# Optimization experiments

Hardware: AMD Instinct MI355X
Metric: run time of the kernel (lower is better)

## Reference

```python
import jax, jax.numpy as jnp
import numpy as np

EMBED_DIM = 1024
NUM_HEADS = 16
HEAD_DIM = EMBED_DIM // NUM_HEADS
BATCH = 4
SEQ = 2048


def setup_inputs() -> dict:
    key = jax.random.key(0)
    ks = jax.random.split(key, 9)
    s = 1.0 / np.sqrt(EMBED_DIM)
    return {
        "query": jax.random.normal(ks[0], (BATCH, SEQ, EMBED_DIM), jnp.float32),
        "Wq": jax.random.normal(ks[1], (EMBED_DIM, EMBED_DIM), jnp.float32) * s,
        "bq": jnp.zeros((EMBED_DIM,), jnp.float32),
        "Wk": jax.random.normal(ks[2], (EMBED_DIM, EMBED_DIM), jnp.float32) * s,
        "bk": jnp.zeros((EMBED_DIM,), jnp.float32),
        "Wv": jax.random.normal(ks[3], (EMBED_DIM, EMBED_DIM), jnp.float32) * s,
        "bv": jnp.zeros((EMBED_DIM,), jnp.float32),
        "Wo": jax.random.normal(ks[4], (EMBED_DIM, EMBED_DIM), jnp.float32) * s,
        "bo": jnp.zeros((EMBED_DIM,), jnp.float32),
    }


def reference(query, Wq, bq, Wk, bk, Wv, bv, Wo, bo):
    bsz, seq, embed_dim = query.shape
    scaling = HEAD_DIM ** (-0.5)
    # projections (torch Linear: x @ W.T + b)
    q = (query @ Wq.T + bq) * scaling
    k = query @ Wk.T + bk
    v = query @ Wv.T + bv
    # [b, h, s, d]
    q = q.reshape(bsz, seq, NUM_HEADS, HEAD_DIM).transpose(0, 2, 1, 3)
    k = k.reshape(bsz, seq, NUM_HEADS, HEAD_DIM).transpose(0, 2, 1, 3)
    v = v.reshape(bsz, seq, NUM_HEADS, HEAD_DIM).transpose(0, 2, 1, 3)
    # full [b, h, s, s] scores (faithful to the naive original)
    scores = jnp.einsum("bhqd,bhkd->bhqk", q, k)
    causal = jnp.tril(jnp.ones((seq, seq), bool))  # [s, s]
    scores = jnp.where(causal[None, None], scores, -jnp.inf)
    probs = jax.nn.softmax(scores, axis=-1)
    attn = jnp.einsum("bhqk,bhkd->bhqd", probs, v)
    attn = attn.transpose(0, 2, 1, 3).reshape(bsz, seq, embed_dim)
    return attn @ Wo.T + bo
```

## Files before the change

### kernel.cpp

```cpp
#include <hip/hip_runtime.h>
#include <stdint.h>

typedef unsigned short u16;
typedef __attribute__((ext_vector_type(8))) __bf16 bf16x8;
typedef __attribute__((ext_vector_type(4))) float f32x4;

#define SEQL 2048
#define NHEADS 16
#define HDIM 64
#define BSZ 4
#define EMB 1024
#define MROWS (BSZ * SEQL)

__device__ __forceinline__ u16 f2bf(float f) {
  union { float f; uint32_t u; } v; v.f = f;
  return (u16)((v.u + 0x7fffu + ((v.u >> 16) & 1u)) >> 16);
}

__device__ __forceinline__ void gload_lds16(const u16* g, u16* l) {
  __builtin_amdgcn_global_load_lds(
      (__attribute__((address_space(1))) void*)(g),
      (__attribute__((address_space(3))) void*)(l), 16, 0, 0);
}

__device__ __forceinline__ void cvt8(const float* __restrict__ in, u16* __restrict__ out, int i) {
  float4 a = *(const float4*)(in + i);
  float4 b = *(const float4*)(in + i + 4);
  uint4 o;
  o.x = f2bf(a.x) | ((uint32_t)f2bf(a.y) << 16);
  o.y = f2bf(a.z) | ((uint32_t)f2bf(a.w) << 16);
  o.z = f2bf(b.x) | ((uint32_t)f2bf(b.y) << 16);
  o.w = f2bf(b.z) | ((uint32_t)f2bf(b.w) << 16);
  *(uint4*)(out + i) = o;
}

__global__ void cvt_kernel(const float* __restrict__ in, u16* __restrict__ out, int n) {
  int i = (blockIdx.x * blockDim.x + threadIdx.x) * 8;
  if (i + 8 <= n) cvt8(in, out, i);
}

__global__ void cvt_w4(const float* __restrict__ w0, const float* __restrict__ w1,
                       const float* __restrict__ w2, const float* __restrict__ w3,
                       u16* __restrict__ o0, u16* __restrict__ o1,
                       u16* __restrict__ o2, u16* __restrict__ o3) {
  const float* in = blockIdx.y == 0 ? w0 : blockIdx.y == 1 ? w1 : blockIdx.y == 2 ? w2 : w3;
  u16* out = blockIdx.y == 0 ? o0 : blockIdx.y == 1 ? o1 : blockIdx.y == 2 ? o2 : o3;
  int i = (blockIdx.x * blockDim.x + threadIdx.x) * 8;
  cvt8(in, out, i);
}

__device__ __forceinline__ void gemm_core(const u16* __restrict__ A, const u16* __restrict__ B,
                                          int m0, int n0, u16* As, u16* Bs, f32x4 acc[4][4]) {
  const int tid = threadIdx.x;
  const int lane = tid & 63;
  const int wid = tid >> 6;
  const int wm = wid >> 1, wn = wid & 1;
  const int srow = lane >> 2;
  const int scol = (lane & 3) * 8;
  const int lrow = lane & 15;
  const int kg = (lane >> 4) * 8;

  const u16* Ag0 = A + (size_t)(m0 + wid * 32 + srow) * EMB + scol;
  const u16* Bg0 = B + (size_t)(n0 + wid * 32 + srow) * EMB + scol;
  u16* Al0 = As + (wid * 32 + srow) * 32 + scol;
  u16* Bl0 = Bs + (wid * 32 + srow) * 32 + scol;

  for (int k0 = 0; k0 < EMB; k0 += 32) {
    gload_lds16(Ag0 + k0, Al0);
    gload_lds16(Ag0 + k0 + 16 * EMB, Al0 + 16 * 32);
    gload_lds16(Bg0 + k0, Bl0);
    gload_lds16(Bg0 + k0 + 16 * EMB, Bl0 + 16 * 32);
    __syncthreads();
    bf16x8 af[4], bfr[4];
#pragma unroll
    for (int f = 0; f < 4; ++f) {
      af[f]  = *(const bf16x8*)(As + (wm * 64 + f * 16 + lrow) * 32 + kg);
      bfr[f] = *(const bf16x8*)(Bs + (wn * 64 + f * 16 + lrow) * 32 + kg);
    }
#pragma unroll
    for (int fm = 0; fm < 4; ++fm)
#pragma unroll
      for (int fn = 0; fn < 4; ++fn)
        acc[fm][fn] = __builtin_amdgcn_mfma_f32_16x16x32_bf16(af[fm], bfr[fn], acc[fm][fn], 0, 0, 0);
    __syncthreads();
  }
}

__global__ __launch_bounds__(256, 2) void gemm_qkv(
    const u16* __restrict__ X,
    const u16* __restrict__ Wq, const u16* __restrict__ Wk, const u16* __restrict__ Wv,
    const float* __restrict__ bq, const float* __restrict__ bk, const float* __restrict__ bv,
    u16* __restrict__ Qb, u16* __restrict__ Kb, u16* __restrict__ Vt) {
  __shared__ u16 As[128 * 32];
  __shared__ u16 Bs[128 * 32];
  const int which = blockIdx.y;
  const u16* W = which == 0 ? Wq : which == 1 ? Wk : Wv;
  const float* bias = which == 0 ? bq : which == 1 ? bk : bv;

  const int mt = blockIdx.x >> 3, nt = blockIdx.x & 7;
  const f32x4 fzero = {0.f, 0.f, 0.f, 0.f};
  f32x4 acc[4][4];
#pragma unroll
  for (int i = 0; i < 4; ++i)
#pragma unroll
    for (int j = 0; j < 4; ++j) acc[i][j] = fzero;

  gemm_core(X, W, mt * 128, nt * 128, As, Bs, acc);

  const int lane = threadIdx.x & 63;
  const int wid = threadIdx.x >> 6;
  const int wm = wid >> 1, wn = wid & 1;
  const int lrow = lane & 15, g = lane >> 4;

  if (which == 2) {
#pragma unroll
    for (int fm = 0; fm < 4; ++fm)
#pragma unroll
      for (int fn = 0; fn < 4; ++fn) {
        int n = nt * 128 + wn * 64 + fn * 16 + lrow;
        float bs = bias[n];
        int h = n >> 6, d = n & 63;
        int m0 = mt * 128 + wm * 64 + fm * 16 + g * 4;
        int b = m0 >> 11, s = m0 & 2047;
        union { u16 s4[4]; uint2 u; } o;
#pragma unroll
        for (int r = 0; r < 4; ++r) o.s4[r] = f2bf(acc[fm][fn][r] + bs);
        *(uint2*)(Vt + ((size_t)(b * NHEADS + h) * HDIM + d) * SEQL + s) = o.u;
      }
  } else {
    u16* Ob = which == 0 ? Qb : Kb;
    const float scale = which == 0 ? 0.125f : 1.0f;
#pragma unroll
    for (int fm = 0; fm < 4; ++fm)
#pragma unroll
      for (int fn = 0; fn < 4; ++fn) {
        int n = nt * 128 + wn * 64 + fn * 16 + lrow;
        float bs = bias[n];
        int h = n >> 6, d = n & 63;
#pragma unroll
        for (int r = 0; r < 4; ++r) {
          int m = mt * 128 + wm * 64 + fm * 16 + g * 4 + r;
          int b = m >> 11, s = m & 2047;
          float v = (acc[fm][fn][r] + bs) * scale;
          Ob[(size_t)((b * NHEADS + h) * SEQL + s) * HDIM + d] = f2bf(v);
        }
      }
  }
}

__global__ __launch_bounds__(256, 2) void gemm_out(
    const u16* __restrict__ Ain, const u16* __restrict__ Wo,
    const float* __restrict__ bo, float* __restrict__ out) {
  __shared__ u16 As[128 * 32];
  __shared__ u16 Bs[128 * 32];
  const int mt = blockIdx.x >> 3, nt = blockIdx.x & 7;
  const f32x4 fzero = {0.f, 0.f, 0.f, 0.f};
  f32x4 acc[4][4];
#pragma unroll
  for (int i = 0; i < 4; ++i)
#pragma unroll
    for (int j = 0; j < 4; ++j) acc[i][j] = fzero;

  gemm_core(Ain, Wo, mt * 128, nt * 128, As, Bs, acc);

  const int lane = threadIdx.x & 63;
  const int wid = threadIdx.x >> 6;
  const int wm = wid >> 1, wn = wid & 1;
  const int lrow = lane & 15, g = lane >> 4;
#pragma unroll
  for (int fm = 0; fm < 4; ++fm)
#pragma unroll
    for (int fn = 0; fn < 4; ++fn) {
      int n = nt * 128 + wn * 64 + fn * 16 + lrow;
      float bs = bo[n];
#pragma unroll
      for (int r = 0; r < 4; ++r) {
        int m = mt * 128 + wm * 64 + fm * 16 + g * 4 + r;
        out[(size_t)m * EMB + n] = acc[fm][fn][r] + bs;
      }
    }
}

__global__ __launch_bounds__(256, 4) void attn2_kernel(
    const u16* __restrict__ Qb, const u16* __restrict__ Kb, const u16* __restrict__ Vt,
    u16* __restrict__ Ab) {
  __shared__ u16 Ks[2][64 * 72];
  __shared__ u16 Vs[2][64 * 72];

  const int bid = blockIdx.x;
  const int grp = bid >> 6;
  const int bh  = bid & 63;
  const int qt  = (grp & 1) ? (grp >> 1) : (31 - (grp >> 1));
  const int q0  = qt * 64;
  const int NT  = qt + 1;

  const int tid = threadIdx.x, lane = tid & 63, wid = tid >> 6;
  const int lrow = lane & 15, g = lane >> 4, kg = g * 8;

  const u16* Qbh = Qb + (size_t)bh * SEQL * HDIM;
  const u16* Kbh = Kb + (size_t)bh * SEQL * HDIM;
  const u16* Vbh = Vt + (size_t)bh * HDIM * SEQL;

  const int qrow = q0 + wid * 16 + lrow;
  const bf16x8 qf0 = *(const bf16x8*)(Qbh + (size_t)qrow * HDIM + kg);
  const bf16x8 qf1 = *(const bf16x8*)(Qbh + (size_t)qrow * HDIM + 32 + kg);

  const int srow = tid >> 3;
  const int sc8  = (tid & 7) * 8;

  float m_run = -1e30f, l_run = 0.f;
  const f32x4 fzero = {0.f, 0.f, 0.f, 0.f};
  f32x4 accO[4];
#pragma unroll
  for (int d = 0; d < 4; ++d) accO[d] = fzero;

  {
    uint4 k0 = *(const uint4*)(Kbh + (size_t)srow * HDIM + sc8);
    uint4 k1 = *(const uint4*)(Kbh + (size_t)(srow + 32) * HDIM + sc8);
    uint4 v0 = *(const uint4*)(Vbh + (size_t)srow * SEQL + sc8);
    uint4 v1 = *(const uint4*)(Vbh + (size_t)(srow + 32) * SEQL + sc8);
    *(uint4*)(&Ks[0][srow * 72 + sc8]) = k0;
    *(uint4*)(&Ks[0][(srow + 32) * 72 + sc8]) = k1;
    *(uint4*)(&Vs[0][srow * 72 + sc8]) = v0;
    *(uint4*)(&Vs[0][(srow + 32) * 72 + sc8]) = v1;
  }
  __syncthreads();

  const int q_max = q0 + wid * 16 + 15;

  for (int t = 0; t < NT; ++t) {
    const int cur = t & 1;
    const int kv0 = t * 64;
    const bool pf = (t + 1 < NT);
    uint4 k0, k1, v0, v1;
    if (pf) {
      const int kvn = kv0 + 64;
      k0 = *(const uint4*)(Kbh + (size_t)(kvn + srow) * HDIM + sc8);
      k1 = *(const uint4*)(Kbh + (size_t)(kvn + srow + 32) * HDIM + sc8);
      v0 = *(const uint4*)(Vbh + (size_t)srow * SEQL + kvn + sc8);
      v1 = *(const uint4*)(Vbh + (size_t)(srow + 32) * SEQL + kvn + sc8);
    }

    if (kv0 <= q_max) {
      f32x4 sacc[4];
#pragma unroll
      for (int kb = 0; kb < 4; ++kb) {
        bf16x8 kfa = *(const bf16x8*)(&Ks[cur][(kb * 16 + lrow) * 72 + kg]);
        bf16x8 kfb = *(const bf16x8*)(&Ks[cur][(kb * 16 + lrow) * 72 + 32 + kg]);
        f32x4 z = fzero;
        z = __builtin_amdgcn_mfma_f32_16x16x32_bf16(kfa, qf0, z, 0, 0, 0);
        z = __builtin_amdgcn_mfma_f32_16x16x32_bf16(kfb, qf1, z, 0, 0, 0);
        sacc[kb] = z;
      }

      if (kv0 + 63 > q0 + wid * 16) {
#pragma unroll
        for (int kb = 0; kb < 4; ++kb)
#pragma unroll
          for (int r = 0; r < 4; ++r)
            if (kv0 + kb * 16 + g * 4 + r > qrow) sacc[kb][r] = -1e30f;
      }

      float mx = sacc[0][0];
#pragma unroll
      for (int kb = 0; kb < 4; ++kb)
#pragma unroll
        for (int r = 0; r < 4; ++r) mx = fmaxf(mx, sacc[kb][r]);
      mx = fmaxf(mx, __shfl_xor(mx, 16));
      mx = fmaxf(mx, __shfl_xor(mx, 32));
      const float mnew = fmaxf(m_run, mx);
      const float sc = __expf(m_run - mnew);
      m_run = mnew;
      l_run *= sc;
#pragma unroll
      for (int d = 0; d < 4; ++d) accO[d] *= sc;

      bf16x8 pa[2];
      float ls = 0.f;
#pragma unroll
      for (int kb = 0; kb < 4; ++kb)
#pragma unroll
        for (int r = 0; r < 4; ++r) {
          float p = __expf(sacc[kb][r] - mnew);
          ls += p;
          pa[kb >> 1][(kb & 1) * 4 + r] = (__bf16)p;
        }
      l_run += ls;

#pragma unroll
      for (int ks = 0; ks < 2; ++ks)
#pragma unroll
        for (int d = 0; d < 4; ++d) {
          const u16* vb = &Vs[cur][(d * 16 + lrow) * 72 + ks * 32 + g * 4];
          union { ushort4 h[2]; bf16x8 v; } vf;
          vf.h[0] = *(const ushort4*)(vb);
          vf.h[1] = *(const ushort4*)(vb + 16);
          accO[d] = __builtin_amdgcn_mfma_f32_16x16x32_bf16(vf.v, pa[ks], accO[d], 0, 0, 0);
        }
    }

    if (pf) {
      const int nb = cur ^ 1;
      *(uint4*)(&Ks[nb][srow * 72 + sc8]) = k0;
      *(uint4*)(&Ks[nb][(srow + 32) * 72 + sc8]) = k1;
      *(uint4*)(&Vs[nb][srow * 72 + sc8]) = v0;
      *(uint4*)(&Vs[nb][(srow + 32) * 72 + sc8]) = v1;
    }
    __syncthreads();
  }

  float l = l_run;
  l += __shfl_xor(l, 16);
  l += __shfl_xor(l, 32);
  const float inv = 1.f / l;
  const int b = bh >> 4, h = bh & 15;
#pragma unroll
  for (int d = 0; d < 4; ++d) {
    union { u16 s4[4]; uint2 u; } o;
#pragma unroll
    for (int r = 0; r < 4; ++r) o.s4[r] = f2bf(accO[d][r] * inv);
    *(uint2*)(Ab + (size_t)(b * SEQL + qrow) * EMB + h * HDIM + d * 16 + g * 4) = o.u;
  }
}

extern "C" void kernel_launch(void* const* d_in, const int* in_sizes, int n_in,
                              void* d_out, int out_size, void* d_ws, size_t ws_size,
                              hipStream_t stream) {
  (void)in_sizes; (void)n_in; (void)out_size; (void)ws_size;
  const float* query = (const float*)d_in[0];
  const float* Wq = (const float*)d_in[1];
  const float* bq = (const float*)d_in[2];
  const float* Wk = (const float*)d_in[3];
  const float* bk = (const float*)d_in[4];
  const float* Wv = (const float*)d_in[5];
  const float* bv = (const float*)d_in[6];
  const float* Wo = (const float*)d_in[7];
  const float* bo = (const float*)d_in[8];
  float* out = (float*)d_out;

  const size_t MB = 1u << 20;
  char* ws = (char*)d_ws;
  u16* Xb  = (u16*)(ws);
  u16* Wqb = (u16*)(ws + 16 * MB);
  u16* Wkb = (u16*)(ws + 18 * MB);
  u16* Wvb = (u16*)(ws + 20 * MB);
  u16* Wob = (u16*)(ws + 22 * MB);
  u16* Qbf = (u16*)(ws + 24 * MB);
  u16* Kbf = (u16*)(ws + 40 * MB);
  u16* Vtg = (u16*)(ws + 56 * MB);
  u16* Ab  = Xb;

  cvt_kernel<<<4096, 256, 0, stream>>>(query, Xb, MROWS * EMB);
  cvt_w4<<<dim3(512, 4), 256, 0, stream>>>(Wq, Wk, Wv, Wo, Wqb, Wkb, Wvb, Wob);
  gemm_qkv<<<dim3(512, 3), 256, 0, stream>>>(Xb, Wqb, Wkb, Wvb, bq, bk, bv, Qbf, Kbf, Vtg);
  attn2_kernel<<<2048, 256, 0, stream>>>(Qbf, Kbf, Vtg, Ab);
  gemm_out<<<512, 256, 0, stream>>>(Ab, Wob, bo, out);
}
```

Measured before the change: 191.4 us.

## Swizzle attention LDS tiles, use exp2 with folded log2e, lazy rescale, setprio

Replaces the padded 72-element LDS rows for K and V with an unpadded 64-element layout using an XOR swizzle, to avoid bank conflicts without padding. Folds log2(e) into the Q scaling so softmax can use the hardware exp2 directly. Skips the running-max rescale unless some lane's max grows by more than 8, which saves multiplies but lets intermediate values grow up to 2^8. It also raises wave priority around the MFMA blocks and drops the per-wave skip of fully masked tiles, so every wave now runs every tile.

```diff
diff --git a/kernel.cpp b/kernel.cpp
--- a/kernel.cpp
+++ b/kernel.cpp
@@ -11,6 +11,7 @@
 #define BSZ 4
 #define EMB 1024
 #define MROWS (BSZ * SEQL)
+#define LOG2E 1.44269504088896f
 
 __device__ __forceinline__ u16 f2bf(float f) {
   union { float f; uint32_t u; } v; v.f = f;
@@ -129,7 +130,7 @@
       }
   } else {
     u16* Ob = which == 0 ? Qb : Kb;
-    const float scale = which == 0 ? 0.125f : 1.0f;
+    const float scale = which == 0 ? 0.125f * LOG2E : 1.0f;
 #pragma unroll
     for (int fm = 0; fm < 4; ++fm)
 #pragma unroll
@@ -181,11 +182,15 @@
     }
 }
 
+__device__ __forceinline__ int swz(int row, int colE) {
+  return row * 64 + (colE ^ ((row & 7) << 3));
+}
+
 __global__ __launch_bounds__(256, 4) void attn2_kernel(
     const u16* __restrict__ Qb, const u16* __restrict__ Kb, const u16* __restrict__ Vt,
     u16* __restrict__ Ab) {
-  __shared__ u16 Ks[2][64 * 72];
-  __shared__ u16 Vs[2][64 * 72];
+  __shared__ u16 Ks[2][64 * 64];
+  __shared__ u16 Vs[2][64 * 64];
 
   const int bid = blockIdx.x;
   const int grp = bid >> 6;
@@ -206,7 +211,7 @@
   const bf16x8 qf1 = *(const bf16x8*)(Qbh + (size_t)qrow * HDIM + 32 + kg);
 
   const int srow = tid >> 3;
-  const int sc8  = (tid & 7) * 8;
+  const int sce  = (tid & 7) * 8;
 
   float m_run = -1e30f, l_run = 0.f;
   const f32x4 fzero = {0.f, 0.f, 0.f, 0.f};
@@ -215,18 +220,16 @@
   for (int d = 0; d < 4; ++d) accO[d] = fzero;
 
   {
-    uint4 k0 = *(const uint4*)(Kbh + (size_t)srow * HDIM + sc8);
-    uint4 k1 = *(const uint4*)(Kbh + (size_t)(srow + 32) * HDIM + sc8);
-    uint4 v0 = *(const uint4*)(Vbh + (size_t)srow * SEQL + sc8);
-    uint4 v1 = *(const uint4*)(Vbh + (size_t)(srow + 32) * SEQL + sc8);
-    *(uint4*)(&Ks[0][srow * 72 + sc8]) = k0;
-    *(uint4*)(&Ks[0][(srow + 32) * 72 + sc8]) = k1;
-    *(uint4*)(&Vs[0][srow * 72 + sc8]) = v0;
-    *(uint4*)(&Vs[0][(srow + 32) * 72 + sc8]) = v1;
+    uint4 k0 = *(const uint4*)(Kbh + (size_t)srow * HDIM + sce);
+    uint4 k1 = *(const uint4*)(Kbh + (size_t)(srow + 32) * HDIM + sce);
+    uint4 v0 = *(const uint4*)(Vbh + (size_t)srow * SEQL + sce);
+    uint4 v1 = *(const uint4*)(Vbh + (size_t)(srow + 32) * SEQL + sce);
+    *(uint4*)(&Ks[0][swz(srow, sce)]) = k0;
+    *(uint4*)(&Ks[0][swz(srow + 32, sce)]) = k1;
+    *(uint4*)(&Vs[0][swz(srow, sce)]) = v0;
+    *(uint4*)(&Vs[0][swz(srow + 32, sce)]) = v1;
   }
   __syncthreads();
-
-  const int q_max = q0 + wid * 16 + 15;
 
   for (int t = 0; t < NT; ++t) {
     const int cur = t & 1;
@@ -235,76 +238,80 @@
     uint4 k0, k1, v0, v1;
     if (pf) {
       const int kvn = kv0 + 64;
-      k0 = *(const uint4*)(Kbh + (size_t)(kvn + srow) * HDIM + sc8);
-      k1 = *(const uint4*)(Kbh + (size_t)(kvn + srow + 32) * HDIM + sc8);
-      v0 = *(const uint4*)(Vbh + (size_t)srow * SEQL + kvn + sc8);
-      v1 = *(const uint4*)(Vbh + (size_t)(srow + 32) * SEQL + kvn + sc8);
-    }
-
-    if (kv0 <= q_max) {
-      f32x4 sacc[4];
-#pragma unroll
-      for (int kb = 0; kb < 4; ++kb) {
-        bf16x8 kfa = *(const bf16x8*)(&Ks[cur][(kb * 16 + lrow) * 72 + kg]);
-        bf16x8 kfb = *(const bf16x8*)(&Ks[cur][(kb * 16 + lrow) * 72 + 32 + kg]);
-        f32x4 z = fzero;
-        z = __builtin_amdgcn_mfma_f32_16x16x32_bf16(kfa, qf0, z, 0, 0, 0);
-        z = __builtin_amdgcn_mfma_f32_16x16x32_bf16(kfb, qf1, z, 0, 0, 0);
-        sacc[kb] = z;
-      }
-
-      if (kv0 + 63 > q0 + wid * 16) {
-#pragma unroll
-        for (int kb = 0; kb < 4; ++kb)
-#pragma unroll
-          for (int r = 0; r < 4; ++r)
-            if (kv0 + kb * 16 + g * 4 + r > qrow) sacc[kb][r] = -1e30f;
-      }
-
-      float mx = sacc[0][0];
+      k0 = *(const uint4*)(Kbh + (size_t)(kvn + srow) * HDIM + sce);
+      k1 = *(const uint4*)(Kbh + (size_t)(kvn + srow + 32) * HDIM + sce);
+      v0 = *(const uint4*)(Vbh + (size_t)srow * SEQL + kvn + sce);
+      v1 = *(const uint4*)(Vbh + (size_t)(srow + 32) * SEQL + kvn + sce);
+    }
+
+    f32x4 sacc[4];
+    __builtin_amdgcn_s_setprio(1);
+#pragma unroll
+    for (int kb = 0; kb < 4; ++kb) {
+      bf16x8 kfa = *(const bf16x8*)(&Ks[cur][swz(kb * 16 + lrow, kg)]);
+      bf16x8 kfb = *(const bf16x8*)(&Ks[cur][swz(kb * 16 + lrow, 32 + kg)]);
+      f32x4 z = fzero;
+      z = __builtin_amdgcn_mfma_f32_16x16x32_bf16(kfa, qf0, z, 0, 0, 0);
+      z = __builtin_amdgcn_mfma_f32_16x16x32_bf16(kfb, qf1, z, 0, 0, 0);
+      sacc[kb] = z;
+    }
+    __builtin_amdgcn_s_setprio(0);
+
+    if (kv0 + 63 > q0 + wid * 16) {
 #pragma unroll
       for (int kb = 0; kb < 4; ++kb)
 #pragma unroll
-        for (int r = 0; r < 4; ++r) mx = fmaxf(mx, sacc[kb][r]);
-      mx = fmaxf(mx, __shfl_xor(mx, 16));
-      mx = fmaxf(mx, __shfl_xor(mx, 32));
+        for (int r = 0; r < 4; ++r)
+          if (kv0 + kb * 16 + g * 4 + r > qrow) sacc[kb][r] = -1e30f;
+    }
+
+    float mx = sacc[0][0];
+#pragma unroll
+    for (int kb = 0; kb < 4; ++kb)
+#pragma unroll
+      for (int r = 0; r < 4; ++r) mx = fmaxf(mx, sacc[kb][r]);
+    mx = fmaxf(mx, __shfl_xor(mx, 16));
+    mx = fmaxf(mx, __shfl_xor(mx, 32));
+
+    if (!__all(mx <= m_run + 8.f)) {
       const float mnew = fmaxf(m_run, mx);
-      const float sc = __expf(m_run - mnew);
+      const float sc = __builtin_amdgcn_exp2f(m_run - mnew);
       m_run = mnew;
       l_run *= sc;
 #pragma unroll
       for (int d = 0; d < 4; ++d) accO[d] *= sc;
-
-      bf16x8 pa[2];
-      float ls = 0.f;
-#pragma unroll
-      for (int kb = 0; kb < 4; ++kb)
-#pragma unroll
-        for (int r = 0; r < 4; ++r) {
-          float p = __expf(sacc[kb][r] - mnew);
-          ls += p;
-          pa[kb >> 1][(kb & 1) * 4 + r] = (__bf16)p;
-        }
-      l_run += ls;
-
-#pragma unroll
-      for (int ks = 0; ks < 2; ++ks)
-#pragma unroll
-        for (int d = 0; d < 4; ++d) {
-          const u16* vb = &Vs[cur][(d * 16 + lrow) * 72 + ks * 32 + g * 4];
-          union { ushort4 h[2]; bf16x8 v; } vf;
-          vf.h[0] = *(const ushort4*)(vb);
-          vf.h[1] = *(const ushort4*)(vb + 16);
-          accO[d] = __builtin_amdgcn_mfma_f32_16x16x32_bf16(vf.v, pa[ks], accO[d], 0, 0, 0);
-        }
-    }
+    }
+
+    bf16x8 pa[2];
+    float ls = 0.f;
+#pragma unroll
+    for (int kb = 0; kb < 4; ++kb)
+#pragma unroll
+      for (int r = 0; r < 4; ++r) {
+        float p = __builtin_amdgcn_exp2f(sacc[kb][r] - m_run);
+        ls += p;
+        pa[kb >> 1][(kb & 1) * 4 + r] = (__bf16)p;
+      }
+    l_run += ls;
+
+    __builtin_amdgcn_s_setprio(1);
+#pragma unroll
+    for (int ks = 0; ks < 2; ++ks)
+#pragma unroll
+      for (int d = 0; d < 4; ++d) {
+        union { ushort4 h[2]; bf16x8 v; } vf;
+        vf.h[0] = *(const ushort4*)(&Vs[cur][swz(d * 16 + lrow, ks * 32 + g * 4)]);
+        vf.h[1] = *(const ushort4*)(&Vs[cur][swz(d * 16 + lrow, ks * 32 + 16 + g * 4)]);
+        accO[d] = __builtin_amdgcn_mfma_f32_16x16x32_bf16(vf.v, pa[ks], accO[d], 0, 0, 0);
+      }
+    __builtin_amdgcn_s_setprio(0);
 
     if (pf) {
       const int nb = cur ^ 1;
-      *(uint4*)(&Ks[nb][srow * 72 + sc8]) = k0;
-      *(uint4*)(&Ks[nb][(srow + 32) * 72 + sc8]) = k1;
-      *(uint4*)(&Vs[nb][srow * 72 + sc8]) = v0;
-      *(uint4*)(&Vs[nb][(srow + 32) * 72 + sc8]) = v1;
+      *(uint4*)(&Ks[nb][swz(srow, sce)]) = k0;
+      *(uint4*)(&Ks[nb][swz(srow + 32, sce)]) = k1;
+      *(uint4*)(&Vs[nb][swz(srow, sce)]) = v0;
+      *(uint4*)(&Vs[nb][swz(srow + 32, sce)]) = v1;
     }
     __syncthreads();
   }
```

New measurement: 191.7 us. About the same (+0.2%).
